# Kernel tuning notes

Measured on AMD Instinct MI355X. Metric: run time of the kernel, lower is better.

Reference implementation:

```python
import jax, jax.numpy as jnp
import numpy as np

B, S, D_IN, D_OUT = 4, 2048, 1024, 1024

def setup_inputs() -> dict:
    key = jax.random.key(0)
    k1, k2, k3, k4, k5, k6 = jax.random.split(key, 6)
    return {
        "inputs_for_keys": jax.random.normal(k1, (B, S, D_IN), dtype=jnp.float32),
        "inputs_for_values": jax.random.normal(k2, (B, S, D_IN), dtype=jnp.float32),
        "inputs_for_queries": jax.random.normal(k3, (B, S, D_IN), dtype=jnp.float32),
        "WK": jax.random.truncated_normal(k4, -2.0, 2.0, (D_IN, D_OUT), dtype=jnp.float32) * 0.1,
        "WV": jax.random.truncated_normal(k5, -2.0, 2.0, (D_IN, D_OUT), dtype=jnp.float32) * 0.1,
        "WQ": jax.random.truncated_normal(k6, -2.0, 2.0, (D_IN, D_OUT), dtype=jnp.float32) * 0.1,
    }

def reference(inputs_for_keys, inputs_for_values, inputs_for_queries, WK, WV, WQ):
    # projections: [B,S,D_in] @ [D_in,D_out] -> [B,S,D_out]
    K = jnp.einsum('bsd,de->bse', inputs_for_keys, WK)
    V = jnp.einsum('bsd,de->bse', inputs_for_values, WV)
    Q = jnp.einsum('bsd,de->bse', inputs_for_queries, WQ)
    # scores: [B,S,S]. NOTE: original TF code scales by sqrt(K.shape[1]) = sqrt(seq_len),
    # not sqrt(head_dim) — reproduce that faithfully.
    scale = jnp.sqrt(jnp.float32(K.shape[1]))
    scores = jnp.einsum('bqe,bke->bqk', Q, K) / scale
    attn = jax.nn.softmax(scores, axis=-1)
    return jnp.einsum('bqk,bke->bqe', attn, V)
```

## Files before the change

### kernel.cpp

```cpp
#include <hip/hip_runtime.h>
#include <hip/hip_bf16.h>


typedef __attribute__((ext_vector_type(4))) float    f32x4;
typedef __attribute__((ext_vector_type(8))) _Float16 f16x8;
typedef __attribute__((ext_vector_type(4))) _Float16 f16x4;

constexpr size_t MiB = 1u << 20;
constexpr size_t MK  = (size_t)8192 * 1024;
constexpr size_t WSZ = (size_t)1024 * 1024;

__device__ __forceinline__ void gload_lds16(const void* g, void* l) {
  __builtin_amdgcn_global_load_lds(
      (const __attribute__((address_space(1))) unsigned int*)g,
      (__attribute__((address_space(3))) unsigned int*)l, 16, 0, 0);
}

#define MFMA16(a, b, c) __builtin_amdgcn_mfma_f32_16x16x32_f16(a, b, c, 0, 0, 0)

__device__ __forceinline__ void swz_block(int& bx, int& by, int& bz) {
  unsigned gx = gridDim.x, gy = gridDim.y;
  unsigned flat = blockIdx.x + gx * (blockIdx.y + gy * blockIdx.z);
  unsigned total = gx * gy * gridDim.z;
  unsigned cpx = total >> 3;
  unsigned s = (flat & 7) * cpx + (flat >> 3);
  bx = s % gx; s /= gx; by = s % gy; bz = s / gy;
}

__global__ __launch_bounds__(256) void convert_x(
    const float* __restrict__ x0, const float* __restrict__ x1,
    const float* __restrict__ x2, _Float16* __restrict__ XF)
{
  const int z = blockIdx.z;
  const float* x = z == 0 ? x0 : (z == 1 ? x1 : x2);
  size_t i = ((size_t)blockIdx.x * 256 + threadIdx.x) * 4;
  float4 v = *(const float4*)(x + i);
  f16x4 h = {(_Float16)v.x, (_Float16)v.y, (_Float16)v.z, (_Float16)v.w};
  *(f16x4*)(XF + (size_t)z * MK + i) = h;
}

__global__ __launch_bounds__(256) void transpose_conv_w(
    const float* __restrict__ w0, const float* __restrict__ w1,
    const float* __restrict__ w2, _Float16* __restrict__ WT)
{
  const int z = blockIdx.z;
  const float* W = z == 0 ? w0 : (z == 1 ? w1 : w2);
  _Float16* o = WT + (size_t)z * WSZ;
  __shared__ float tile[32][33];
  const int bx = blockIdx.x * 32;
  const int by = blockIdx.y * 32;
  const int tx = threadIdx.x & 31, ty = threadIdx.x >> 5;
  #pragma unroll
  for (int r = 0; r < 32; r += 8)
    tile[ty + r][tx] = W[(size_t)(by + ty + r) * 1024 + bx + tx];
  __syncthreads();
  #pragma unroll
  for (int r = 0; r < 32; r += 8)
    o[(size_t)(bx + ty + r) * 1024 + by + tx] = (_Float16)tile[tx][ty + r];
}

__global__ __launch_bounds__(256) void transpose_v(
    const _Float16* __restrict__ V, _Float16* __restrict__ Vt)
{
  const _Float16* v = V + (size_t)blockIdx.z * 2048 * 1024;
  _Float16* o = Vt + (size_t)blockIdx.z * 1024 * 2048;
  __shared__ _Float16 tile[32][33];
  const int bx = blockIdx.x * 32;
  const int by = blockIdx.y * 32;
  const int tx = threadIdx.x & 31, ty = threadIdx.x >> 5;
  #pragma unroll
  for (int r = 0; r < 32; r += 8)
    tile[ty + r][tx] = v[(size_t)(by + ty + r) * 1024 + bx + tx];
  __syncthreads();
  #pragma unroll
  for (int r = 0; r < 32; r += 8)
    o[(size_t)(bx + ty + r) * 2048 + by + tx] = tile[tx][ty + r];
}

template <int MODE>
__global__ __launch_bounds__(512, 2) void gemm8p(
    const _Float16* __restrict__ At, size_t sA,
    const _Float16* __restrict__ Bt, size_t sB,
    void* __restrict__ Cv, size_t sCz,
    int N, int K, float scale)
{
  extern __shared__ char lds[];
  int bx, by, bz;
  swz_block(bx, by, bz);
  const _Float16* A = At + (size_t)bz * sA;
  const _Float16* B = Bt + (size_t)bz * sB;

  const int gm0 = by * 256, gn0 = bx * 256;
  const int tid = threadIdx.x;
  const int lane = tid & 63, wave = tid >> 6;
  const int wm = (wave >> 2) * 128;
  const int wn = (wave & 3) * 64;
  const int fr = lane & 15, fq = lane >> 4;
  const int nkt = K >> 6;

  const int clog = ((tid & 7) ^ ((tid >> 3) & 7)) * 8;
  const _Float16* srcA = A + (size_t)(gm0 + (tid >> 3)) * K + clog;
  const _Float16* srcB = B + (size_t)(gn0 + (tid >> 3)) * K + clog;
  char* const dst0 = lds + tid * 16;

  auto SH = [&](int tile, int h) {
    const _Float16* s = (h < 2 ? srcA : srcB) + (size_t)((h & 1) * 128) * K
                        + tile * 64;
    char* d = dst0 + (tile & 1) * 65536 + h * 16384;
    gload_lds16(s, d);
    gload_lds16(s + (size_t)64 * K, d + 8192);
  };

  const int axor = fr & 7;
  const int pc0 = (fq ^ axor) * 16;
  const int pc1 = ((4 + fq) ^ axor) * 16;
  const int arb = (wm + fr) * 128;
  const int brb = 32768 + (wn + fr) * 128;

  f32x4 acc[8][4] = {};
  f16x8 af[4][2], b0[2][2], b1[2][2];

  SH(0, 0); SH(0, 1); SH(0, 2); SH(0, 3);
  if (nkt > 1) {
    SH(1, 0);
    asm volatile("s_waitcnt vmcnt(2)" ::: "memory");
  } else {
    asm volatile("s_waitcnt vmcnt(0)" ::: "memory");
  }
  __builtin_amdgcn_s_barrier();
  __builtin_amdgcn_sched_barrier(0);

#define PHASE_MID                                          \
  __builtin_amdgcn_s_barrier();                            \
  asm volatile("s_waitcnt lgkmcnt(0)" ::: "memory");       \
  __builtin_amdgcn_sched_barrier(0);                       \
  __builtin_amdgcn_s_setprio(1);
#define PHASE_END                                          \
  __builtin_amdgcn_s_setprio(0);                           \
  __builtin_amdgcn_sched_barrier(0);                       \
  __builtin_amdgcn_s_barrier();

  for (int t = 0; t < nkt; ++t) {
    const char* buf = lds + (t & 1) * 65536;
    const bool st1 = (t + 1) < nkt;

    #pragma unroll
    for (int mi = 0; mi < 4; ++mi) {
      af[mi][0] = *(const f16x8*)(buf + arb + mi * 2048 + pc0);
      af[mi][1] = *(const f16x8*)(buf + arb + mi * 2048 + pc1);
    }
    #pragma unroll
    for (int ni = 0; ni < 2; ++ni) {
      b0[ni][0] = *(const f16x8*)(buf + brb + ni * 2048 + pc0);
      b0[ni][1] = *(const f16x8*)(buf + brb + ni * 2048 + pc1);
    }
    if (st1) SH(t + 1, 1);
    PHASE_MID
    #pragma unroll
    for (int mi = 0; mi < 4; ++mi)
      #pragma unroll
      for (int ni = 0; ni < 2; ++ni)
        #pragma unroll
        for (int kk = 0; kk < 2; ++kk)
          acc[mi][ni] = MFMA16(af[mi][kk], b0[ni][kk], acc[mi][ni]);
    PHASE_END

    #pragma unroll
    for (int ni = 0; ni < 2; ++ni) {
      b1[ni][0] = *(const f16x8*)(buf + brb + (ni + 2) * 2048 + pc0);
      b1[ni][1] = *(const f16x8*)(buf + brb + (ni + 2) * 2048 + pc1);
    }
    if (st1) SH(t + 1, 2);
    PHASE_MID
    #pragma unroll
    for (int mi = 0; mi < 4; ++mi)
      #pragma unroll
      for (int ni = 0; ni < 2; ++ni)
        #pragma unroll
        for (int kk = 0; kk < 2; ++kk)
          acc[mi][ni + 2] = MFMA16(af[mi][kk], b1[ni][kk], acc[mi][ni + 2]);
    PHASE_END

    #pragma unroll
    for (int mi = 0; mi < 4; ++mi) {
      af[mi][0] = *(const f16x8*)(buf + arb + (mi + 4) * 2048 + pc0);
      af[mi][1] = *(const f16x8*)(buf + arb + (mi + 4) * 2048 + pc1);
    }
    if (st1) SH(t + 1, 3);
    PHASE_MID
    #pragma unroll
    for (int mi = 0; mi < 4; ++mi)
      #pragma unroll
      for (int ni = 0; ni < 2; ++ni)
        #pragma unroll
        for (int kk = 0; kk < 2; ++kk)
          acc[mi + 4][ni] = MFMA16(af[mi][kk], b0[ni][kk], acc[mi + 4][ni]);
    PHASE_END

    const bool st2 = (t + 2) < nkt;
    if (st2) SH(t + 2, 0);
    __builtin_amdgcn_s_barrier();
    __builtin_amdgcn_s_setprio(1);
    #pragma unroll
    for (int mi = 0; mi < 4; ++mi)
      #pragma unroll
      for (int ni = 0; ni < 2; ++ni)
        #pragma unroll
        for (int kk = 0; kk < 2; ++kk)
          acc[mi + 4][ni + 2] = MFMA16(af[mi][kk], b1[ni][kk], acc[mi + 4][ni + 2]);
    __builtin_amdgcn_s_setprio(0);
    __builtin_amdgcn_sched_barrier(0);
    if (st2) asm volatile("s_waitcnt vmcnt(2)" ::: "memory");
    else     asm volatile("s_waitcnt vmcnt(0)" ::: "memory");
    __builtin_amdgcn_s_barrier();
  }
#undef PHASE_MID
#undef PHASE_END

  const int erow = gm0 + wm + fq * 4;
  const int ecol = gn0 + wn + fr;
  #pragma unroll
  for (int m = 0; m < 8; ++m)
    #pragma unroll
    for (int n = 0; n < 4; ++n) {
      size_t base = (size_t)(erow + m * 16) * N + (ecol + n * 16);
      #pragma unroll
      for (int r = 0; r < 4; ++r) {
        float v = acc[m][n][r];
        if constexpr (MODE == 0)
          ((float*)Cv + (size_t)bz * sCz)[base + (size_t)r * N] = v * scale;
        else if constexpr (MODE == 1)
          ((_Float16*)Cv + (size_t)bz * sCz)[base + (size_t)r * N] = (_Float16)v;
        else
          ((_Float16*)Cv + (size_t)bz * sCz)[base + (size_t)r * N] =
              (_Float16)(v * scale);
      }
    }
}

template <int MODE>
__global__ __launch_bounds__(512, 2) void gemm256(
    const _Float16* __restrict__ At, size_t sA,
    const _Float16* __restrict__ Bt, size_t sB,
    void* __restrict__ C0v, size_t sCz,
    int N, int K, float scale)
{
  extern __shared__ char lds[];
  constexpr int BB = 128 * 64;
  char* ldsAb = lds;
  char* ldsBb = lds + 65536;

  int bx, by, bz;
  swz_block(bx, by, bz);
  const _Float16* A = At + (size_t)bz * sA;
  const _Float16* B = Bt + (size_t)bz * sB;

  const int gm0 = by * 256;
  const int gn0 = bx * 128;
  const int tid = threadIdx.x;
  const int lane = tid & 63, wave = tid >> 6;
  const int wm = (wave >> 1) * 64;
  const int wn = (wave & 1) * 64;
  const int fr = lane & 15, fq = lane >> 4;

  const int nkt = K >> 5;

  const int cbs = (((tid & 3) ^ ((tid >> 3) & 3)) << 4);
  const size_t aOff = (size_t)(gm0 + (tid >> 2)) * K + (cbs >> 1);
  const size_t bOff = (size_t)(gn0 + (tid >> 2)) * K + (cbs >> 1);
  const int cbr  = (fq * 16) ^ (((fr >> 1) & 3) << 4);
  const int arow = (wm + fr) * 64 + cbr;
  const int brow = (wn + fr) * 64 + cbr;

  f32x4 acc[4][4] = {};

  for (int tp = 0; tp < 3; ++tp) {
    const _Float16* gA = A + aOff + tp * 32;
    const _Float16* gB = B + bOff + tp * 32;
    char* dA = ldsAb + tp * 16384 + tid * 16;
    char* dB = ldsBb + tp * BB + tid * 16;
    gload_lds16(gA, dA);
    gload_lds16(gA + (size_t)128 * K, dA + 8192);
    gload_lds16(gB, dB);
  }
  asm volatile("s_waitcnt vmcnt(6)" ::: "memory");
  __builtin_amdgcn_s_barrier();
  __builtin_amdgcn_sched_barrier(0);

  for (int t = 0; t < nkt; ++t) {
    const char* pA = ldsAb + (t & 3) * 16384;
    const char* pB = ldsBb + (t & 3) * BB;
    const int tp = t + 3;
    const bool st = tp < nkt;
    const _Float16* gA = A + aOff + (st ? tp : 0) * 32;
    const _Float16* gB = B + bOff + (st ? tp : 0) * 32;
    char* dA = ldsAb + (tp & 3) * 16384 + tid * 16;
    char* dB = ldsBb + (tp & 3) * BB + tid * 16;

    if (st) { gload_lds16(gA, dA); gload_lds16(gB, dB); }
    f16x8 bfr[4], af[2];
    #pragma unroll
    for (int n = 0; n < 4; ++n) bfr[n] = *(const f16x8*)(pB + brow + n * 1024);
    #pragma unroll
    for (int m = 0; m < 2; ++m) af[m] = *(const f16x8*)(pA + arow + m * 1024);
    __builtin_amdgcn_s_setprio(1);
    #pragma unroll
    for (int m = 0; m < 2; ++m)
      #pragma unroll
      for (int n = 0; n < 4; ++n) acc[m][n] = MFMA16(af[m], bfr[n], acc[m][n]);
    __builtin_amdgcn_s_setprio(0);
    __builtin_amdgcn_s_barrier();
    __builtin_amdgcn_sched_barrier(0);

    if (st) gload_lds16(gA + (size_t)128 * K, dA + 8192);
    #pragma unroll
    for (int m = 0; m < 2; ++m) af[m] = *(const f16x8*)(pA + arow + (m + 2) * 1024);
    __builtin_amdgcn_s_setprio(1);
    #pragma unroll
    for (int m = 0; m < 2; ++m)
      #pragma unroll
      for (int n = 0; n < 4; ++n) acc[m + 2][n] = MFMA16(af[m], bfr[n], acc[m + 2][n]);
    __builtin_amdgcn_s_setprio(0);
    asm volatile("s_waitcnt vmcnt(6)" ::: "memory");
    __builtin_amdgcn_s_barrier();
    __builtin_amdgcn_sched_barrier(0);
  }

  const int erow = gm0 + wm + fq * 4;
  const int ecol = gn0 + wn + fr;
  float* C = (float*)C0v + (size_t)bz * sCz;
  #pragma unroll
  for (int m = 0; m < 4; ++m)
    #pragma unroll
    for (int n = 0; n < 4; ++n) {
      size_t base = (size_t)(erow + m * 16) * N + (ecol + n * 16);
      #pragma unroll
      for (int r = 0; r < 4; ++r)
        C[base + (size_t)r * N] = acc[m][n][r] * scale;
    }
}

__global__ __launch_bounds__(256) void softmax_rows(
    const _Float16* __restrict__ S, _Float16* __restrict__ P)
{
  const int w = threadIdx.x >> 6, lane = threadIdx.x & 63;
  const size_t row = (size_t)blockIdx.x * 4 + w;
  const _Float16* sr = S + row * 2048;

  f16x8 v[4];
  #pragma unroll
  for (int c = 0; c < 4; ++c)
    v[c] = *(const f16x8*)(sr + c * 512 + lane * 8);

  float m = -1e30f;
  #pragma unroll
  for (int c = 0; c < 4; ++c)
    #pragma unroll
    for (int j = 0; j < 8; ++j) m = fmaxf(m, (float)v[c][j]);
  #pragma unroll
  for (int o = 32; o >= 1; o >>= 1) m = fmaxf(m, __shfl_xor(m, o));

  float e[4][8];
  float s = 0.f;
  #pragma unroll
  for (int c = 0; c < 4; ++c)
    #pragma unroll
    for (int j = 0; j < 8; ++j) {
      e[c][j] = __expf((float)v[c][j] - m);
      s += e[c][j];
    }
  #pragma unroll
  for (int o = 32; o >= 1; o >>= 1) s += __shfl_xor(s, o);

  const float inv = 1.0f / s;
  _Float16* pr = P + row * 2048;
  #pragma unroll
  for (int c = 0; c < 4; ++c) {
    f16x8 p;
    #pragma unroll
    for (int j = 0; j < 8; ++j) p[j] = (_Float16)(e[c][j] * inv);
    *(f16x8*)(pr + c * 512 + lane * 8) = p;
  }
}

extern "C" void kernel_launch(void* const* d_in, const int* in_sizes, int n_in,
                              void* d_out, int out_size, void* d_ws, size_t ws_size,
                              hipStream_t stream)
{
  const float* Xk = (const float*)d_in[0];
  const float* Xv = (const float*)d_in[1];
  const float* Xq = (const float*)d_in[2];
  const float* WK = (const float*)d_in[3];
  const float* WV = (const float*)d_in[4];
  const float* WQ = (const float*)d_in[5];
  float* out = (float*)d_out;
  char* ws = (char*)d_ws;

  _Float16* XF   = (_Float16*)(ws);
  _Float16* WT   = (_Float16*)(ws + 48 * MiB);
  _Float16* PROJ = (_Float16*)(ws + 54 * MiB);
  _Float16* VT   = (_Float16*)(ws + 102 * MiB);
  _Float16* SC   = (_Float16*)(ws + 118 * MiB);
  _Float16* P    = (_Float16*)(ws);

  _Float16* Kp = PROJ;
  _Float16* Vp = PROJ + MK;
  _Float16* Qp = PROJ + 2 * MK;

  auto* fP  = gemm8p<1>;
  auto* fSC = gemm8p<2>;
  auto* fPV = gemm256<0>;
  (void)hipFuncSetAttribute((const void*)fP,  hipFuncAttributeMaxDynamicSharedMemorySize, 131072);
  (void)hipFuncSetAttribute((const void*)fSC, hipFuncAttributeMaxDynamicSharedMemorySize, 131072);
  (void)hipFuncSetAttribute((const void*)fPV, hipFuncAttributeMaxDynamicSharedMemorySize, 98304);

  convert_x<<<dim3(8192, 1, 3), 256, 0, stream>>>(Xk, Xv, Xq, XF);
  transpose_conv_w<<<dim3(32, 32, 3), 256, 0, stream>>>(WK, WV, WQ, WT);
  gemm8p<1><<<dim3(4, 32, 3), 512, 131072, stream>>>(
      XF, MK, WT, WSZ, PROJ, MK, 1024, 1024, 1.0f);
  transpose_v<<<dim3(32, 64, 4), 256, 0, stream>>>(Vp, VT);
  gemm8p<2><<<dim3(8, 8, 4), 512, 131072, stream>>>(
      Qp, (size_t)2048 * 1024, Kp, (size_t)2048 * 1024,
      SC, (size_t)2048 * 2048, 2048, 1024, 0.022097086912079608f);
  softmax_rows<<<dim3(2048), 256, 0, stream>>>(SC, P);
  gemm256<0><<<dim3(8, 8, 4), 512, 98304, stream>>>(
      P, (size_t)2048 * 2048, VT, (size_t)1024 * 2048,
      out, (size_t)2048 * 1024, 1024, 2048, 1.0f);
}
```

Measured before the change: 202.4 us.

## Rewrite 256x128 GEMM with BK=64 double-buffered pipeline and reuse for projections

```diff
diff --git a/kernel.cpp b/kernel.cpp
--- a/kernel.cpp
+++ b/kernel.cpp
@@ -239,104 +239,135 @@
 }
 
 template <int MODE>
-__global__ __launch_bounds__(512, 2) void gemm256(
+__global__ __launch_bounds__(512, 2) void gemm8pN(
     const _Float16* __restrict__ At, size_t sA,
     const _Float16* __restrict__ Bt, size_t sB,
-    void* __restrict__ C0v, size_t sCz,
+    void* __restrict__ Cv, size_t sCz,
     int N, int K, float scale)
 {
   extern __shared__ char lds[];
-  constexpr int BB = 128 * 64;
-  char* ldsAb = lds;
-  char* ldsBb = lds + 65536;
-
   int bx, by, bz;
   swz_block(bx, by, bz);
   const _Float16* A = At + (size_t)bz * sA;
   const _Float16* B = Bt + (size_t)bz * sB;
 
-  const int gm0 = by * 256;
-  const int gn0 = bx * 128;
+  const int gm0 = by * 256, gn0 = bx * 128;
   const int tid = threadIdx.x;
   const int lane = tid & 63, wave = tid >> 6;
   const int wm = (wave >> 1) * 64;
   const int wn = (wave & 1) * 64;
   const int fr = lane & 15, fq = lane >> 4;
-
-  const int nkt = K >> 5;
-
-  const int cbs = (((tid & 3) ^ ((tid >> 3) & 3)) << 4);
-  const size_t aOff = (size_t)(gm0 + (tid >> 2)) * K + (cbs >> 1);
-  const size_t bOff = (size_t)(gn0 + (tid >> 2)) * K + (cbs >> 1);
-  const int cbr  = (fq * 16) ^ (((fr >> 1) & 3) << 4);
-  const int arow = (wm + fr) * 64 + cbr;
-  const int brow = (wn + fr) * 64 + cbr;
+  const int nkt = K >> 6;
+
+  const int clog = ((tid & 7) ^ ((tid >> 3) & 7)) * 8;
+  const _Float16* srcA = A + (size_t)(gm0 + (tid >> 3)) * K + clog;
+  const _Float16* srcB = B + (size_t)(gn0 + (tid >> 3)) * K + clog;
+  char* const dst0 = lds + tid * 16;
+
+  auto SHU = [&](int tile, int u) {
+    const _Float16* s = (u < 2 ? srcA + (size_t)(u * 128) * K : srcB)
+                        + tile * 64;
+    char* d = dst0 + (tile & 1) * 49152 + u * 16384;
+    gload_lds16(s, d);
+    gload_lds16(s + (size_t)64 * K, d + 8192);
+  };
+
+  const int axor = fr & 7;
+  const int pc0 = (fq ^ axor) * 16;
+  const int pc1 = ((4 + fq) ^ axor) * 16;
+  const int arb = (wm + fr) * 128;
+  const int brb = 32768 + (wn + fr) * 128;
 
   f32x4 acc[4][4] = {};
-
-  for (int tp = 0; tp < 3; ++tp) {
-    const _Float16* gA = A + aOff + tp * 32;
-    const _Float16* gB = B + bOff + tp * 32;
-    char* dA = ldsAb + tp * 16384 + tid * 16;
-    char* dB = ldsBb + tp * BB + tid * 16;
-    gload_lds16(gA, dA);
-    gload_lds16(gA + (size_t)128 * K, dA + 8192);
-    gload_lds16(gB, dB);
+  f16x8 af[4][2], b0[2][2], b1[2][2];
+
+  SHU(0, 0); SHU(0, 1); SHU(0, 2);
+  if (nkt > 1) {
+    SHU(1, 0);
+    asm volatile("s_waitcnt vmcnt(2)" ::: "memory");
+  } else {
+    asm volatile("s_waitcnt vmcnt(0)" ::: "memory");
   }
-  asm volatile("s_waitcnt vmcnt(6)" ::: "memory");
   __builtin_amdgcn_s_barrier();
   __builtin_amdgcn_sched_barrier(0);
 
+#define PHASE_MID                                          \
+  __builtin_amdgcn_s_barrier();                            \
+  asm volatile("s_waitcnt lgkmcnt(0)" ::: "memory");       \
+  __builtin_amdgcn_sched_barrier(0);                       \
+  __builtin_amdgcn_s_setprio(1);
+#define PHASE_END                                          \
+  __builtin_amdgcn_s_setprio(0);                           \
+  __builtin_amdgcn_sched_barrier(0);                       \
+  __builtin_amdgcn_s_barrier();
+
   for (int t = 0; t < nkt; ++t) {
-    const char* pA = ldsAb + (t & 3) * 16384;
-    const char* pB = ldsBb + (t & 3) * BB;
-    const int tp = t + 3;
-    const bool st = tp < nkt;
-    const _Float16* gA = A + aOff + (st ? tp : 0) * 32;
-    const _Float16* gB = B + bOff + (st ? tp : 0) * 32;
-    char* dA = ldsAb + (tp & 3) * 16384 + tid * 16;
-    char* dB = ldsBb + (tp & 3) * BB + tid * 16;
-
-    if (st) { gload_lds16(gA, dA); gload_lds16(gB, dB); }
-    f16x8 bfr[4], af[2];
-    #pragma unroll
-    for (int n = 0; n < 4; ++n) bfr[n] = *(const f16x8*)(pB + brow + n * 1024);
-    #pragma unroll
-    for (int m = 0; m < 2; ++m) af[m] = *(const f16x8*)(pA + arow + m * 1024);
+    const char* buf = lds + (t & 1) * 49152;
+    const bool st1 = (t + 1) < nkt;
+    const bool st2 = (t + 2) < nkt;
+
+    #pragma unroll
+    for (int mi = 0; mi < 4; ++mi) {
+      af[mi][0] = *(const f16x8*)(buf + arb + mi * 2048 + pc0);
+      af[mi][1] = *(const f16x8*)(buf + arb + mi * 2048 + pc1);
+    }
+    #pragma unroll
+    for (int ni = 0; ni < 2; ++ni) {
+      b0[ni][0] = *(const f16x8*)(buf + brb + ni * 2048 + pc0);
+      b0[ni][1] = *(const f16x8*)(buf + brb + ni * 2048 + pc1);
+    }
+    if (st1) { SHU(t + 1, 1); SHU(t + 1, 2); }
+    PHASE_MID
+    #pragma unroll
+    for (int mi = 0; mi < 4; ++mi)
+      #pragma unroll
+      for (int ni = 0; ni < 2; ++ni)
+        #pragma unroll
+        for (int kk = 0; kk < 2; ++kk)
+          acc[mi][ni] = MFMA16(af[mi][kk], b0[ni][kk], acc[mi][ni]);
+    PHASE_END
+
+    #pragma unroll
+    for (int ni = 0; ni < 2; ++ni) {
+      b1[ni][0] = *(const f16x8*)(buf + brb + (ni + 2) * 2048 + pc0);
+      b1[ni][1] = *(const f16x8*)(buf + brb + (ni + 2) * 2048 + pc1);
+    }
+    if (st2) SHU(t + 2, 0);
+    __builtin_amdgcn_s_barrier();
+    asm volatile("s_waitcnt lgkmcnt(0)" ::: "memory");
+    __builtin_amdgcn_sched_barrier(0);
     __builtin_amdgcn_s_setprio(1);
     #pragma unroll
-    for (int m = 0; m < 2; ++m)
-      #pragma unroll
-      for (int n = 0; n < 4; ++n) acc[m][n] = MFMA16(af[m], bfr[n], acc[m][n]);
+    for (int mi = 0; mi < 4; ++mi)
+      #pragma unroll
+      for (int ni = 0; ni < 2; ++ni)
+        #pragma unroll
+        for (int kk = 0; kk < 2; ++kk)
+          acc[mi][ni + 2] = MFMA16(af[mi][kk], b1[ni][kk], acc[mi][ni + 2]);
     __builtin_amdgcn_s_setprio(0);
+    __builtin_amdgcn_sched_barrier(0);
+    if (st2)      asm volatile("s_waitcnt vmcnt(2)" ::: "memory");
+    else          asm volatile("s_waitcnt vmcnt(0)" ::: "memory");
     __builtin_amdgcn_s_barrier();
-    __builtin_amdgcn_sched_barrier(0);
-
-    if (st) gload_lds16(gA + (size_t)128 * K, dA + 8192);
-    #pragma unroll
-    for (int m = 0; m < 2; ++m) af[m] = *(const f16x8*)(pA + arow + (m + 2) * 1024);
-    __builtin_amdgcn_s_setprio(1);
-    #pragma unroll
-    for (int m = 0; m < 2; ++m)
-      #pragma unroll
-      for (int n = 0; n < 4; ++n) acc[m + 2][n] = MFMA16(af[m], bfr[n], acc[m + 2][n]);
-    __builtin_amdgcn_s_setprio(0);
-    asm volatile("s_waitcnt vmcnt(6)" ::: "memory");
-    __builtin_amdgcn_s_barrier();
-    __builtin_amdgcn_sched_barrier(0);
   }
+#undef PHASE_MID
+#undef PHASE_END
 
   const int erow = gm0 + wm + fq * 4;
   const int ecol = gn0 + wn + fr;
-  float* C = (float*)C0v + (size_t)bz * sCz;
   #pragma unroll
   for (int m = 0; m < 4; ++m)
     #pragma unroll
     for (int n = 0; n < 4; ++n) {
       size_t base = (size_t)(erow + m * 16) * N + (ecol + n * 16);
       #pragma unroll
-      for (int r = 0; r < 4; ++r)
-        C[base + (size_t)r * N] = acc[m][n][r] * scale;
+      for (int r = 0; r < 4; ++r) {
+        float v = acc[m][n][r];
+        if constexpr (MODE == 0)
+          ((float*)Cv + (size_t)bz * sCz)[base + (size_t)r * N] = v * scale;
+        else
+          ((_Float16*)Cv + (size_t)bz * sCz)[base + (size_t)r * N] = (_Float16)v;
+      }
     }
 }
 
@@ -407,23 +438,23 @@
   _Float16* Vp = PROJ + MK;
   _Float16* Qp = PROJ + 2 * MK;
 
-  auto* fP  = gemm8p<1>;
+  auto* fP  = gemm8pN<1>;
   auto* fSC = gemm8p<2>;
-  auto* fPV = gemm256<0>;
-  (void)hipFuncSetAttribute((const void*)fP,  hipFuncAttributeMaxDynamicSharedMemorySize, 131072);
+  auto* fPV = gemm8pN<0>;
+  (void)hipFuncSetAttribute((const void*)fP,  hipFuncAttributeMaxDynamicSharedMemorySize, 98304);
   (void)hipFuncSetAttribute((const void*)fSC, hipFuncAttributeMaxDynamicSharedMemorySize, 131072);
   (void)hipFuncSetAttribute((const void*)fPV, hipFuncAttributeMaxDynamicSharedMemorySize, 98304);
 
   convert_x<<<dim3(8192, 1, 3), 256, 0, stream>>>(Xk, Xv, Xq, XF);
   transpose_conv_w<<<dim3(32, 32, 3), 256, 0, stream>>>(WK, WV, WQ, WT);
-  gemm8p<1><<<dim3(4, 32, 3), 512, 131072, stream>>>(
+  gemm8pN<1><<<dim3(8, 32, 3), 512, 98304, stream>>>(
       XF, MK, WT, WSZ, PROJ, MK, 1024, 1024, 1.0f);
   transpose_v<<<dim3(32, 64, 4), 256, 0, stream>>>(Vp, VT);
   gemm8p<2><<<dim3(8, 8, 4), 512, 131072, stream>>>(
       Qp, (size_t)2048 * 1024, Kp, (size_t)2048 * 1024,
       SC, (size_t)2048 * 2048, 2048, 1024, 0.022097086912079608f);
   softmax_rows<<<dim3(2048), 256, 0, stream>>>(SC, P);
-  gemm256<0><<<dim3(8, 8, 4), 512, 98304, stream>>>(
+  gemm8pN<0><<<dim3(8, 8, 4), 512, 98304, stream>>>(
       P, (size_t)2048 * 2048, VT, (size_t)1024 * 2048,
       out, (size_t)2048 * 1024, 1024, 2048, 1.0f);
 }
```

After: 197.4 us. 1.03x faster.
